# Kernel optimization log

Measured on AMD Instinct MI355X. Metric: run time of the kernel, lower is better.

The kernel has to match this reference:

```python
import jax, jax.numpy as jnp
import numpy as np

N = 100000
E = 1600000
H = 8
D_IN = 128
D_HEAD = 16  # output_dim // n_heads


def setup_inputs() -> dict:
    key = jax.random.key(0)
    ks = jax.random.split(key, 8)
    x = jax.random.normal(ks[0], (N, D_IN), dtype=jnp.float32)
    W = jax.random.normal(ks[1], (H, D_IN, D_HEAD), dtype=jnp.float32) * 0.05
    a1 = jax.random.normal(ks[2], (H, D_HEAD), dtype=jnp.float32) * 0.1
    b1 = jnp.zeros((H,), dtype=jnp.float32)
    a2 = jax.random.normal(ks[3], (H, D_HEAD), dtype=jnp.float32) * 0.1
    b2 = jnp.zeros((H,), dtype=jnp.float32)
    src = jnp.sort(jax.random.randint(ks[4], (E,), 0, N)).astype(jnp.int32)
    dst = jax.random.randint(ks[5], (E,), 0, N).astype(jnp.int32)
    return {"x": x, "W": W, "a1": a1, "b1": b1, "a2": a2, "b2": b2,
            "src": src, "dst": dst}


def _gat_forward(x, W, a1, b1, a2, b2, src, dst):
    n = x.shape[0]
    # per-head linear transform: [H, N, D_HEAD]
    feats = jnp.einsum('nd,hdo->hno', x, W)
    # per-node attention scalars (1x1 conv with bias): [H, N]
    f1 = jnp.einsum('hno,ho->hn', feats, a1) + b1[:, None]
    f2 = jnp.einsum('hno,ho->hn', feats, a2) + b2[:, None]
    # edge logits: logit[e] = f1[src[e]] + f2[dst[e]]  -> [E, H]
    e = f1[:, src].T + f2[:, dst].T
    e = jnp.maximum(0.2 * e, e)  # leaky_relu
    # sparse row-softmax over each source node's neighbors (segment softmax)
    m = jax.ops.segment_max(e, src, num_segments=n)           # [N, H]
    ex = jnp.exp(e - m[src])                                   # [E, H]
    denom = jax.ops.segment_sum(ex, src, num_segments=n)      # [N, H]
    coef = ex / denom[src]                                     # [E, H]
    # spmm: out[i] = sum_{j in N(i)} coef[ij] * feats[j]
    feats_nhd = jnp.transpose(feats, (1, 0, 2))                # [N, H, D_HEAD]
    msg = coef[:, :, None] * feats_nhd[dst]                    # [E, H, D_HEAD]
    out = jax.ops.segment_sum(msg, src, num_segments=n)       # [N, H, D_HEAD]
    out = out.reshape(n, H * D_HEAD)
    return jax.nn.elu(out)


def reference(x, W, a1, b1, a2, b2, src, dst):
    return _gat_forward(x, W, a1, b1, a2, b2, src, dst)
```

## Files before the change

### kernel.cpp

```cpp
#include <hip/hip_runtime.h>
#include <hip/hip_bf16.h>
#include <math.h>

#define HEADS 8
#define D_IN 128
#define D_HEAD 16
#define D_OUT 128

typedef unsigned short ushort_t;
typedef unsigned int uint_t;
typedef __attribute__((ext_vector_type(8))) short short8;
typedef __attribute__((ext_vector_type(4))) float floatx4;

static __device__ inline uint_t f32_to_bf16(float f) {
    uint_t u = __float_as_uint(f);
    return (u + 0x7fffu + ((u >> 16) & 1u)) >> 16;
}
static __device__ inline uint_t pack_bf16(float lo, float hi) {
    return (f32_to_bf16(hi) << 16) | f32_to_bf16(lo);
}
static __device__ inline float bf_lo(uint_t p) { return __uint_as_float(p << 16); }
static __device__ inline float bf_hi(uint_t p) { return __uint_as_float(p & 0xffff0000u); }

#define PREP_WBLOCKS 64
__global__ __launch_bounds__(256) void prep_kernel(
    const float* __restrict__ Wg, ushort_t* __restrict__ Wfrag,
    const int* __restrict__ src, int* __restrict__ row_ptr, int n, int e)
{
    if (blockIdx.x < PREP_WBLOCKS) {
        int t = blockIdx.x * 256 + threadIdx.x;
        int j    = t & 7;
        int lane = (t >> 3) & 63;
        int ks   = (t >> 9) & 3;
        int ct   = t >> 11;
        int k = ks * 32 + (lane >> 4) * 8 + j;
        int m = lane & 15;
        float v = Wg[(size_t)ct * (D_IN * D_HEAD) + k * D_HEAD + m];
        Wfrag[t] = (ushort_t)f32_to_bf16(v);
    } else {
        int i = (blockIdx.x - PREP_WBLOCKS) * 256 + threadIdx.x;
        if (i > e) return;
        int sp = (i == 0) ? -1 : src[i - 1];
        int sc = (i == e) ? n  : src[i];
        for (int node = sp + 1; node <= sc; ++node) row_ptr[node] = i;
    }
}

__global__ __launch_bounds__(256) void gemm_feats_mfma(
    const float* __restrict__ x, const ushort_t* __restrict__ Wfrag,
    const float* __restrict__ a1, const float* __restrict__ b1,
    const float* __restrict__ a2, const float* __restrict__ b2,
    ushort_t* __restrict__ feats, float* __restrict__ f1,
    float* __restrict__ f2, int n)
{
    __shared__ ushort_t Xs[128][136];

    const int tid  = threadIdx.x;
    const int wave = tid >> 6;
    const int lane = tid & 63;
    const int row0 = blockIdx.x * 128;

#pragma unroll
    for (int it = 0; it < 16; ++it) {
        int idx = it * 256 + tid;
        int r   = idx >> 5;
        int c4  = (idx & 31) * 4;
        float4 v = make_float4(0.f, 0.f, 0.f, 0.f);
        if (row0 + r < n) v = *(const float4*)(x + (size_t)(row0 + r) * D_IN + c4);
        *(uint2*)&Xs[r][c4] = make_uint2(pack_bf16(v.x, v.y), pack_bf16(v.z, v.w));
    }
    __syncthreads();

    const int m  = lane & 15;
    const int kg = lane >> 4;

    floatx4 acc[2][8];
#pragma unroll
    for (int nt = 0; nt < 2; ++nt)
#pragma unroll
        for (int ct = 0; ct < 8; ++ct) acc[nt][ct] = (floatx4){0.f, 0.f, 0.f, 0.f};

#pragma unroll
    for (int ks = 0; ks < 4; ++ks) {
        short8 xb0 = *(const short8*)&Xs[wave * 32 + m][ks * 32 + kg * 8];
        short8 xb1 = *(const short8*)&Xs[wave * 32 + 16 + m][ks * 32 + kg * 8];
#pragma unroll
        for (int ct = 0; ct < 8; ++ct) {
            short8 wa = *(const short8*)(Wfrag + ((size_t)(ct * 4 + ks) * 64 + lane) * 8);
            acc[0][ct] = __builtin_amdgcn_mfma_f32_16x16x32_bf16(wa, xb0, acc[0][ct], 0, 0, 0);
            acc[1][ct] = __builtin_amdgcn_mfma_f32_16x16x32_bf16(wa, xb1, acc[1][ct], 0, 0, 0);
        }
    }

#pragma unroll
    for (int nt = 0; nt < 2; ++nt) {
        const int node = row0 + wave * 32 + nt * 16 + m;
        const bool valid = node < n;
        if (valid) {
#pragma unroll
            for (int ct = 0; ct < 8; ++ct) {
                uint_t lo = pack_bf16(acc[nt][ct][0], acc[nt][ct][1]);
                uint_t hi = pack_bf16(acc[nt][ct][2], acc[nt][ct][3]);
                *(uint2*)(feats + (size_t)node * D_OUT + ct * 16 + kg * 4) = make_uint2(lo, hi);
            }
        }
#pragma unroll
        for (int ct = 0; ct < 8; ++ct) {
            float4 A1 = *(const float4*)(a1 + ct * D_HEAD + kg * 4);
            float4 A2 = *(const float4*)(a2 + ct * D_HEAD + kg * 4);
            float p1 = acc[nt][ct][0] * A1.x + acc[nt][ct][1] * A1.y +
                       acc[nt][ct][2] * A1.z + acc[nt][ct][3] * A1.w;
            float p2 = acc[nt][ct][0] * A2.x + acc[nt][ct][1] * A2.y +
                       acc[nt][ct][2] * A2.z + acc[nt][ct][3] * A2.w;
            p1 += __shfl_xor(p1, 16); p1 += __shfl_xor(p1, 32);
            p2 += __shfl_xor(p2, 16); p2 += __shfl_xor(p2, 32);
            if (kg == 0 && valid) {
                f1[(size_t)node * HEADS + ct] = p1 + b1[ct];
                f2[(size_t)node * HEADS + ct] = p2 + b2[ct];
            }
        }
    }
}

__global__ __launch_bounds__(256) void aggregate_kernel(
    const int* __restrict__ row_ptr, const int* __restrict__ dst,
    const ushort_t* __restrict__ feats,
    const float* __restrict__ f1, const float* __restrict__ f2,
    float* __restrict__ out, int n)
{
    int node = blockIdx.x * 4 + (threadIdx.x >> 6);
    node = __builtin_amdgcn_readfirstlane(node);
    if (node >= n) return;
    const int lane = threadIdx.x & 63;
    const int h = lane >> 3;

    const float f1v   = f1[(size_t)node * HEADS + h];
    const int   start = row_ptr[node];
    const int   end   = row_ptr[node + 1];

    const ushort_t* fl = feats + 2 * lane;

    float s = 0.f, ax = 0.f, ay = 0.f;
    int e = start;
    for (; e + 8 <= end; e += 8) {
        int d[8];
#pragma unroll
        for (int q = 0; q < 8; ++q) d[q] = dst[e + q];
        const int   dq = dst[e + (lane & 7)];
        const float g  = f2[(size_t)dq * HEADS + h];
        float z = f1v + g;
        z = fmaxf(z, 0.2f * z);
        const float w = __expf(z);
        uint_t p[8];
#pragma unroll
        for (int q = 0; q < 8; ++q)
            p[q] = *(const uint_t*)(fl + (size_t)d[q] * D_OUT);
#pragma unroll
        for (int q = 0; q < 8; ++q) {
            const float wq = __shfl(w, (lane & 56) | q);
            s += wq;
            ax = fmaf(wq, bf_lo(p[q]), ax);
            ay = fmaf(wq, bf_hi(p[q]), ay);
        }
    }
    for (; e < end; ++e) {
        const int d = dst[e];
        const float g = f2[(size_t)d * HEADS + h];
        const uint_t p = *(const uint_t*)(fl + (size_t)d * D_OUT);
        float z = f1v + g;
        z = fmaxf(z, 0.2f * z);
        const float w = __expf(z);
        s += w;
        ax = fmaf(w, bf_lo(p), ax);
        ay = fmaf(w, bf_hi(p), ay);
    }

    float rx = 0.f, ry = 0.f;
    if (end > start) {
        rx = ax / s;
        ry = ay / s;
        rx = rx > 0.f ? rx : expm1f(rx);
        ry = ry > 0.f ? ry : expm1f(ry);
    }
    *(float2*)(out + (size_t)node * D_OUT + 2 * lane) = make_float2(rx, ry);
}

extern "C" void kernel_launch(void* const* d_in, const int* in_sizes, int n_in,
                              void* d_out, int out_size, void* d_ws, size_t ws_size,
                              hipStream_t stream)
{
    const float* x  = (const float*)d_in[0];
    const float* W  = (const float*)d_in[1];
    const float* a1 = (const float*)d_in[2];
    const float* b1 = (const float*)d_in[3];
    const float* a2 = (const float*)d_in[4];
    const float* b2 = (const float*)d_in[5];
    const int* src  = (const int*)d_in[6];
    const int* dst  = (const int*)d_in[7];
    float* out = (float*)d_out;

    const int n = in_sizes[0] / D_IN;
    const int e = in_sizes[6];

    char* ws = (char*)d_ws;
    size_t off = 0;
    ushort_t* feats = (ushort_t*)(ws + off);
    off += (size_t)n * D_OUT * sizeof(ushort_t); off = (off + 255) & ~(size_t)255;
    float* f1 = (float*)(ws + off);
    off += (size_t)n * HEADS * sizeof(float);    off = (off + 255) & ~(size_t)255;
    float* f2 = (float*)(ws + off);
    off += (size_t)n * HEADS * sizeof(float);    off = (off + 255) & ~(size_t)255;
    int* row_ptr = (int*)(ws + off);
    off += (size_t)(n + 1) * sizeof(int);        off = (off + 255) & ~(size_t)255;
    ushort_t* Wfrag = (ushort_t*)(ws + off);

    dim3 blk(256);
    const int rp_blocks = (e + 1 + 255) / 256;
    prep_kernel<<<dim3(PREP_WBLOCKS + rp_blocks), blk, 0, stream>>>(
        W, Wfrag, src, row_ptr, n, e);
    gemm_feats_mfma<<<dim3((n + 127) / 128), blk, 0, stream>>>(
        x, Wfrag, a1, b1, a2, b2, feats, f1, f2, n);
    aggregate_kernel<<<dim3((n + 3) / 4), blk, 0, stream>>>(
        row_ptr, dst, feats, f1, f2, out, n);
}
```

Before: 217.6 us.

## Store features head-major and aggregate one head per block for locality

Features and attention scalars are now stored head-major ([H, N, 16] and [H, N]). The aggregation kernel is reorganized so each block handles a single head for a chunk of 16 nodes. Each wave processes 8 edges at once, with 8 lanes per edge, and reduces the partial sums with shuffles. The aim is to shrink the per-head gather working set (3.2 MB per head) so it stays cache-resident, at the cost of 32-byte scattered gathers, redundant reads of row_ptr and dst across 8 head-blocks, and lane underutilization for nodes with few edges.

```diff
diff --git a/kernel.cpp b/kernel.cpp
--- a/kernel.cpp
+++ b/kernel.cpp
@@ -101,7 +101,8 @@
             for (int ct = 0; ct < 8; ++ct) {
                 uint_t lo = pack_bf16(acc[nt][ct][0], acc[nt][ct][1]);
                 uint_t hi = pack_bf16(acc[nt][ct][2], acc[nt][ct][3]);
-                *(uint2*)(feats + (size_t)node * D_OUT + ct * 16 + kg * 4) = make_uint2(lo, hi);
+                *(uint2*)(feats + ((size_t)ct * n + node) * D_HEAD + kg * 4) =
+                    make_uint2(lo, hi);
             }
         }
 #pragma unroll
@@ -115,8 +116,8 @@
             p1 += __shfl_xor(p1, 16); p1 += __shfl_xor(p1, 32);
             p2 += __shfl_xor(p2, 16); p2 += __shfl_xor(p2, 32);
             if (kg == 0 && valid) {
-                f1[(size_t)node * HEADS + ct] = p1 + b1[ct];
-                f2[(size_t)node * HEADS + ct] = p2 + b2[ct];
+                f1[(size_t)ct * n + node] = p1 + b1[ct];
+                f2[(size_t)ct * n + node] = p2 + b2[ct];
             }
         }
     }
@@ -128,61 +129,55 @@
     const float* __restrict__ f1, const float* __restrict__ f2,
     float* __restrict__ out, int n)
 {
-    int node = blockIdx.x * 4 + (threadIdx.x >> 6);
-    node = __builtin_amdgcn_readfirstlane(node);
-    if (node >= n) return;
-    const int lane = threadIdx.x & 63;
-    const int h = lane >> 3;
-
-    const float f1v   = f1[(size_t)node * HEADS + h];
-    const int   start = row_ptr[node];
-    const int   end   = row_ptr[node + 1];
-
-    const ushort_t* fl = feats + 2 * lane;
-
-    float s = 0.f, ax = 0.f, ay = 0.f;
-    int e = start;
-    for (; e + 8 <= end; e += 8) {
-        int d[8];
-#pragma unroll
-        for (int q = 0; q < 8; ++q) d[q] = dst[e + q];
-        const int   dq = dst[e + (lane & 7)];
-        const float g  = f2[(size_t)dq * HEADS + h];
-        float z = f1v + g;
-        z = fmaxf(z, 0.2f * z);
-        const float w = __expf(z);
-        uint_t p[8];
-#pragma unroll
-        for (int q = 0; q < 8; ++q)
-            p[q] = *(const uint_t*)(fl + (size_t)d[q] * D_OUT);
-#pragma unroll
-        for (int q = 0; q < 8; ++q) {
-            const float wq = __shfl(w, (lane & 56) | q);
-            s += wq;
-            ax = fmaf(wq, bf_lo(p[q]), ax);
-            ay = fmaf(wq, bf_hi(p[q]), ay);
-        }
-    }
-    for (; e < end; ++e) {
-        const int d = dst[e];
-        const float g = f2[(size_t)d * HEADS + h];
-        const uint_t p = *(const uint_t*)(fl + (size_t)d * D_OUT);
-        float z = f1v + g;
-        z = fmaxf(z, 0.2f * z);
-        const float w = __expf(z);
-        s += w;
-        ax = fmaf(w, bf_lo(p), ax);
-        ay = fmaf(w, bf_hi(p), ay);
-    }
-
-    float rx = 0.f, ry = 0.f;
-    if (end > start) {
-        rx = ax / s;
-        ry = ay / s;
-        rx = rx > 0.f ? rx : expm1f(rx);
-        ry = ry > 0.f ? ry : expm1f(ry);
-    }
-    *(float2*)(out + (size_t)node * D_OUT + 2 * lane) = make_float2(rx, ry);
+    const int hh    = blockIdx.x & 7;
+    const int chunk = blockIdx.x >> 3;
+    const int wave  = threadIdx.x >> 6;
+    const int lane  = threadIdx.x & 63;
+    const int q     = lane >> 3;
+    const int cp    = lane & 7;
+
+    const float*    f1h = f1 + (size_t)hh * n;
+    const float*    f2h = f2 + (size_t)hh * n;
+    const ushort_t* fh  = feats + (size_t)hh * n * D_HEAD + cp * 2;
+
+#pragma unroll
+    for (int i = 0; i < 4; ++i) {
+        const int node = chunk * 16 + wave * 4 + i;
+        if (node >= n) break;
+        const int start = row_ptr[node];
+        const int end   = row_ptr[node + 1];
+        const float f1v = f1h[node];
+
+        float s = 0.f, ax = 0.f, ay = 0.f;
+        for (int e = start; e < end; e += 8) {
+            const int rem = end - e;
+            const int qq  = (q < rem) ? q : rem - 1;
+            const int d   = dst[e + qq];
+            const float g = f2h[d];
+            float z = f1v + g;
+            z = fmaxf(z, 0.2f * z);
+            const float w = (q < rem) ? __expf(z) : 0.f;
+            const uint_t p = *(const uint_t*)(fh + (size_t)d * D_HEAD);
+            s += w;
+            ax = fmaf(w, bf_lo(p), ax);
+            ay = fmaf(w, bf_hi(p), ay);
+        }
+        s  += __shfl_xor(s, 8);  s  += __shfl_xor(s, 16);  s  += __shfl_xor(s, 32);
+        ax += __shfl_xor(ax, 8); ax += __shfl_xor(ax, 16); ax += __shfl_xor(ax, 32);
+        ay += __shfl_xor(ay, 8); ay += __shfl_xor(ay, 16); ay += __shfl_xor(ay, 32);
+
+        if (q == 0) {
+            float rx = 0.f, ry = 0.f;
+            if (end > start) {
+                rx = ax / s;
+                ry = ay / s;
+                rx = rx > 0.f ? rx : expm1f(rx);
+                ry = ry > 0.f ? ry : expm1f(ry);
+            }
+            *(float2*)(out + (size_t)node * D_OUT + hh * D_HEAD + cp * 2) =
+                make_float2(rx, ry);
+        }
+    }
 }
 
 extern "C" void kernel_launch(void* const* d_in, const int* in_sizes, int n_in,
@@ -205,13 +200,13 @@
     char* ws = (char*)d_ws;
     size_t off = 0;
     ushort_t* feats = (ushort_t*)(ws + off);
-    off += (size_t)n * D_OUT * sizeof(ushort_t); off = (off + 255) & ~(size_t)255;
+    off += (size_t)HEADS * n * D_HEAD * sizeof(ushort_t); off = (off + 255) & ~(size_t)255;
     float* f1 = (float*)(ws + off);
-    off += (size_t)n * HEADS * sizeof(float);    off = (off + 255) & ~(size_t)255;
+    off += (size_t)HEADS * n * sizeof(float);             off = (off + 255) & ~(size_t)255;
     float* f2 = (float*)(ws + off);
-    off += (size_t)n * HEADS * sizeof(float);    off = (off + 255) & ~(size_t)255;
+    off += (size_t)HEADS * n * sizeof(float);             off = (off + 255) & ~(size_t)255;
     int* row_ptr = (int*)(ws + off);
-    off += (size_t)(n + 1) * sizeof(int);        off = (off + 255) & ~(size_t)255;
+    off += (size_t)(n + 1) * sizeof(int);                 off = (off + 255) & ~(size_t)255;
     ushort_t* Wfrag = (ushort_t*)(ws + off);
 
     dim3 blk(256);
@@ -220,6 +215,7 @@
         W, Wfrag, src, row_ptr, n, e);
     gemm_feats_mfma<<<dim3((n + 127) / 128), blk, 0, stream>>>(
         x, Wfrag, a1, b1, a2, b2, feats, f1, f2, n);
-    aggregate_kernel<<<dim3((n + 3) / 4), blk, 0, stream>>>(
+    const int node_chunks = (n + 15) / 16;
+    aggregate_kernel<<<dim3(8 * node_chunks), blk, 0, stream>>>(
         row_ptr, dst, feats, f1, f2, out, n);
 }
```

New measurement: 386.5 us. +77.6%, slower.

## Fold attention vectors into W as extra MFMA tile and stage weights in LDS

Applied to the files above, without the earlier changes.

Precomputes W·a1 and W·a2 per head in the prep kernel as a ninth 16-column weight tile, so the GEMM produces f1/f2 directly from x through one extra MFMA instead of shuffle reductions over the head outputs. Weight fragments are copied into shared memory once per block, and the tile per block shrinks from 128 to 64 rows (one 16-row tile per wave), doubling the block count. f1/f2 are now computed from bf16-rounded folded weights rather than from the fp32 accumulators, which changes numerics slightly. The larger LDS footprint (~54KB) may reduce occupancy.

```diff
diff --git a/kernel.cpp b/kernel.cpp
--- a/kernel.cpp
+++ b/kernel.cpp
@@ -24,11 +24,15 @@
 
 #define PREP_WBLOCKS 64
 __global__ __launch_bounds__(256) void prep_kernel(
-    const float* __restrict__ Wg, ushort_t* __restrict__ Wfrag,
+    const float* __restrict__ Wg,
+    const float* __restrict__ a1, const float* __restrict__ a2,
+    ushort_t* __restrict__ Wfrag,
     const int* __restrict__ src, int* __restrict__ row_ptr, int n, int e)
 {
-    if (blockIdx.x < PREP_WBLOCKS) {
-        int t = blockIdx.x * 256 + threadIdx.x;
+    const int rp_blocks = (e + 1 + 255) / 256;
+    const int bid = blockIdx.x;
+    if (bid < PREP_WBLOCKS) {
+        int t = bid * 256 + threadIdx.x;
         int j    = t & 7;
         int lane = (t >> 3) & 63;
         int ks   = (t >> 9) & 3;
@@ -37,31 +41,54 @@
         int m = lane & 15;
         float v = Wg[(size_t)ct * (D_IN * D_HEAD) + k * D_HEAD + m];
         Wfrag[t] = (ushort_t)f32_to_bf16(v);
-    } else {
-        int i = (blockIdx.x - PREP_WBLOCKS) * 256 + threadIdx.x;
+    } else if (bid < PREP_WBLOCKS + rp_blocks) {
+        int i = (bid - PREP_WBLOCKS) * 256 + threadIdx.x;
         if (i > e) return;
         int sp = (i == 0) ? -1 : src[i - 1];
         int sc = (i == e) ? n  : src[i];
         for (int node = sp + 1; node <= sc; ++node) row_ptr[node] = i;
+    } else {
+#pragma unroll
+        for (int i = 0; i < 8; ++i) {
+            int t = i * 256 + threadIdx.x;
+            int j  = t & 7;
+            int ln = (t >> 3) & 63;
+            int ks = (t >> 9) & 3;
+            int k  = ks * 32 + (ln >> 4) * 8 + j;
+            int mm = ln & 15;
+            int h  = mm & 7;
+            const float* wrow = Wg + (size_t)h * (D_IN * D_HEAD) + k * D_HEAD;
+            const float* av   = (mm < 8 ? a1 : a2) + h * D_HEAD;
+            float s = 0.f;
+#pragma unroll
+            for (int o = 0; o < D_HEAD; ++o) s = fmaf(wrow[o], av[o], s);
+            Wfrag[8 * 2048 + t] = (ushort_t)f32_to_bf16(s);
+        }
     }
 }
 
 __global__ __launch_bounds__(256) void gemm_feats_mfma(
     const float* __restrict__ x, const ushort_t* __restrict__ Wfrag,
-    const float* __restrict__ a1, const float* __restrict__ b1,
-    const float* __restrict__ a2, const float* __restrict__ b2,
+    const float* __restrict__ b1, const float* __restrict__ b2,
     ushort_t* __restrict__ feats, float* __restrict__ f1,
     float* __restrict__ f2, int n)
 {
-    __shared__ ushort_t Xs[128][136];
+    __shared__ ushort_t Xs[64][136];
+    __shared__ ushort_t WsF[9 * 2048];
 
     const int tid  = threadIdx.x;
     const int wave = tid >> 6;
     const int lane = tid & 63;
-    const int row0 = blockIdx.x * 128;
-
-#pragma unroll
-    for (int it = 0; it < 16; ++it) {
+    const int row0 = blockIdx.x * 64;
+
+    {
+        const uint4* wsrc = (const uint4*)Wfrag;
+        uint4*       wdst = (uint4*)WsF;
+#pragma unroll
+        for (int i = 0; i < 9; ++i) wdst[i * 256 + tid] = wsrc[i * 256 + tid];
+    }
+#pragma unroll
+    for (int it = 0; it < 8; ++it) {
         int idx = it * 256 + tid;
         int r   = idx >> 5;
         int c4  = (idx & 31) * 4;
@@ -74,51 +101,34 @@
     const int m  = lane & 15;
     const int kg = lane >> 4;
 
-    floatx4 acc[2][8];
-#pragma unroll
-    for (int nt = 0; nt < 2; ++nt)
-#pragma unroll
-        for (int ct = 0; ct < 8; ++ct) acc[nt][ct] = (floatx4){0.f, 0.f, 0.f, 0.f};
+    floatx4 acc[9];
+#pragma unroll
+    for (int ct = 0; ct < 9; ++ct) acc[ct] = (floatx4){0.f, 0.f, 0.f, 0.f};
 
 #pragma unroll
     for (int ks = 0; ks < 4; ++ks) {
-        short8 xb0 = *(const short8*)&Xs[wave * 32 + m][ks * 32 + kg * 8];
-        short8 xb1 = *(const short8*)&Xs[wave * 32 + 16 + m][ks * 32 + kg * 8];
+        short8 xb = *(const short8*)&Xs[wave * 16 + m][ks * 32 + kg * 8];
+#pragma unroll
+        for (int ct = 0; ct < 9; ++ct) {
+            short8 wa = *(const short8*)&WsF[((ct * 4 + ks) * 64 + lane) * 8];
+            acc[ct] = __builtin_amdgcn_mfma_f32_16x16x32_bf16(wa, xb, acc[ct], 0, 0, 0);
+        }
+    }
+
+    const int node = row0 + wave * 16 + m;
+    if (node < n) {
 #pragma unroll
         for (int ct = 0; ct < 8; ++ct) {
-            short8 wa = *(const short8*)(Wfrag + ((size_t)(ct * 4 + ks) * 64 + lane) * 8);
-            acc[0][ct] = __builtin_amdgcn_mfma_f32_16x16x32_bf16(wa, xb0, acc[0][ct], 0, 0, 0);
-            acc[1][ct] = __builtin_amdgcn_mfma_f32_16x16x32_bf16(wa, xb1, acc[1][ct], 0, 0, 0);
-        }
-    }
-
-#pragma unroll
-    for (int nt = 0; nt < 2; ++nt) {
-        const int node = row0 + wave * 32 + nt * 16 + m;
-        const bool valid = node < n;
-        if (valid) {
-#pragma unroll
-            for (int ct = 0; ct < 8; ++ct) {
-                uint_t lo = pack_bf16(acc[nt][ct][0], acc[nt][ct][1]);
-                uint_t hi = pack_bf16(acc[nt][ct][2], acc[nt][ct][3]);
-                *(uint2*)(feats + (size_t)node * D_OUT + ct * 16 + kg * 4) = make_uint2(lo, hi);
-            }
-        }
-#pragma unroll
-        for (int ct = 0; ct < 8; ++ct) {
-            float4 A1 = *(const float4*)(a1 + ct * D_HEAD + kg * 4);
-            float4 A2 = *(const float4*)(a2 + ct * D_HEAD + kg * 4);
-            float p1 = acc[nt][ct][0] * A1.x + acc[nt][ct][1] * A1.y +
-                       acc[nt][ct][2] * A1.z + acc[nt][ct][3] * A1.w;
-            float p2 = acc[nt][ct][0] * A2.x + acc[nt][ct][1] * A2.y +
-                       acc[nt][ct][2] * A2.z + acc[nt][ct][3] * A2.w;
-            p1 += __shfl_xor(p1, 16); p1 += __shfl_xor(p1, 32);
-            p2 += __shfl_xor(p2, 16); p2 += __shfl_xor(p2, 32);
-            if (kg == 0 && valid) {
-                f1[(size_t)node * HEADS + ct] = p1 + b1[ct];
-                f2[(size_t)node * HEADS + ct] = p2 + b2[ct];
-            }
-        }
+            uint_t lo = pack_bf16(acc[ct][0], acc[ct][1]);
+            uint_t hi = pack_bf16(acc[ct][2], acc[ct][3]);
+            *(uint2*)(feats + (size_t)node * D_OUT + ct * 16 + kg * 4) = make_uint2(lo, hi);
+        }
+        const float* bb = (kg < 2) ? b1 : b2;
+        float4 bv = *(const float4*)(bb + (kg & 1) * 4);
+        float4 o = make_float4(acc[8][0] + bv.x, acc[8][1] + bv.y,
+                               acc[8][2] + bv.z, acc[8][3] + bv.w);
+        float* dstp = ((kg < 2) ? f1 : f2) + (size_t)node * HEADS + (kg & 1) * 4;
+        *(float4*)dstp = o;
     }
 }
 
@@ -216,10 +226,10 @@
 
     dim3 blk(256);
     const int rp_blocks = (e + 1 + 255) / 256;
-    prep_kernel<<<dim3(PREP_WBLOCKS + rp_blocks), blk, 0, stream>>>(
-        W, Wfrag, src, row_ptr, n, e);
-    gemm_feats_mfma<<<dim3((n + 127) / 128), blk, 0, stream>>>(
-        x, Wfrag, a1, b1, a2, b2, feats, f1, f2, n);
+    prep_kernel<<<dim3(PREP_WBLOCKS + rp_blocks + 1), blk, 0, stream>>>(
+        W, a1, a2, Wfrag, src, row_ptr, n, e);
+    gemm_feats_mfma<<<dim3((n + 63) / 64), blk, 0, stream>>>(
+        x, Wfrag, b1, b2, feats, f1, f2, n);
     aggregate_kernel<<<dim3((n + 3) / 4), blk, 0, stream>>>(
         row_ptr, dst, feats, f1, f2, out, n);
 }
```

New measurement: 216.7 us. About the same (-0.4%).
